# Kernel tuning notes

Hardware: AMD Instinct MI355X
Metric: run time of the kernel (lower is better)

## Reference

```python
import jax, jax.numpy as jnp
import numpy as np

B, T, D, V = 2, 2048, 768, 50257
REWARD_SCALE = 0.5
DIV_WEIGHT = 0.1
EPS = 1e-8  # torch cosine_similarity eps


def setup_inputs() -> dict:
    key = jax.random.key(0)
    k1, k2, k3, k4 = jax.random.split(key, 4)
    return {
        "pass2_hidden": jax.random.normal(k1, (B, T, D), dtype=jnp.float32),
        "pass3_hidden": jax.random.normal(k2, (B, T, D), dtype=jnp.float32),
        "W": jax.random.normal(k3, (V, D), dtype=jnp.float32) * 0.02,  # lm_head weight [V, D]
        "targets": jax.random.randint(k4, (B, T), 0, V, dtype=jnp.int64),
    }


def _masked_ce(hidden, W, targets):
    # hidden: [B,T,D], W: [V,D], targets: [B,T] with ignore_index=-1
    logits = jnp.einsum('btd,vd->btv', hidden, W).reshape(B * T, V)
    t = targets.reshape(B * T)
    valid = t != -1
    safe_t = jnp.where(valid, t, 0)
    logp = jax.nn.log_softmax(logits, axis=-1)
    nll = -jnp.take_along_axis(logp, safe_t[:, None], axis=-1)[:, 0]
    nll = jnp.where(valid, nll, 0.0)
    return nll.sum() / jnp.maximum(valid.sum(), 1).astype(nll.dtype)


def reference(pass2_hidden, pass3_hidden, W, targets):
    # pass 2 CE computed under no_grad in the original
    loss_p2 = jax.lax.stop_gradient(_masked_ce(pass2_hidden, W, targets))
    loss_p3 = _masked_ce(pass3_hidden, W, targets)
    reward_loss = -REWARD_SCALE * (loss_p2 - loss_p3)

    p2 = jax.lax.stop_gradient(pass2_hidden.reshape(B * T, D))  # .detach()
    p3 = pass3_hidden.reshape(B * T, D)
    n2 = jnp.maximum(jnp.linalg.norm(p2, axis=-1), EPS)
    n3 = jnp.maximum(jnp.linalg.norm(p3, axis=-1), EPS)
    cos = jnp.sum(p2 * p3, axis=-1) / (n2 * n3)
    divergence_loss = DIV_WEIGHT * cos.mean()
    return reward_loss + divergence_loss
```

## Files before the change

### kernel.cpp

```cpp
#include <hip/hip_runtime.h>
#include <math.h>

#define BT     4096
#define M_TOT  8192
#define KDIM   768
#define VDIM   50257
#define NBLK   393
#define NB256  197
#define KCH    24
#define KT     12
#define REWARD_SCALE 0.5
#define DIV_WEIGHT   0.1
#define EPS_COS      1e-8f
#define LOG2E        1.44269504088896340736f

typedef _Float16 half8 __attribute__((ext_vector_type(8)));
typedef float    f32x4 __attribute__((ext_vector_type(4)));

#define A_FRAGS (64*KCH*8*64)
#define W_FRAGS (NBLK*KCH*8*64)

__device__ __forceinline__ void g2l16(const short* g, short* l) {
    __builtin_amdgcn_global_load_lds(
        (const __attribute__((address_space(1))) unsigned int*)(const void*)g,
        (__attribute__((address_space(3))) unsigned int*)(void*)l,
        16, 0, 0);
}

__global__ __launch_bounds__(256)
void convert_A_kernel(const float* __restrict__ p2, const float* __restrict__ p3,
                      short* __restrict__ Ahi)
{
    __shared__ float Ls[128][36];
    const int mb = blockIdx.x;
    const int k0 = blockIdx.y;
    const int tid = threadIdx.x;

#pragma unroll
    for (int p = 0; p < 4; ++p) {
        int i = p * 1024 + tid * 4;
        int r = i >> 5;
        int c = i & 31;
        int m = mb * 128 + r;
        const float* src = (m < BT) ? (p2 + (size_t)m * KDIM)
                                    : (p3 + (size_t)(m - BT) * KDIM);
        float4 v = *(const float4*)(src + k0 * 32 + c);
        *(float4*)&Ls[r][c] = v;
    }
    __syncthreads();

    size_t base = ((size_t)(mb * KCH + k0) * 8) * 64;
#pragma unroll
    for (int h = 0; h < 2; ++h) {
        int f    = tid + h * 256;
        int lane = f & 63;
        int tile = f >> 6;
        int row  = tile * 16 + (lane & 15);
        int kq   = (lane >> 4) * 8;
        half8 out;
#pragma unroll
        for (int j = 0; j < 8; ++j) out[j] = (_Float16)Ls[row][kq + j];
        *(half8*)(Ahi + (base + f) * 8) = out;
    }
}

__global__ __launch_bounds__(256)
void convert_W_kernel(const float* __restrict__ W, short* __restrict__ Whi)
{
    __shared__ float Ls[128][36];
    const int nb = blockIdx.x;
    const int k0 = blockIdx.y;
    const int tid = threadIdx.x;

#pragma unroll
    for (int p = 0; p < 4; ++p) {
        int i = p * 1024 + tid * 4;
        int r = i >> 5;
        int c = i & 31;
        int v = nb * 128 + r;
        float4 val = make_float4(0.f, 0.f, 0.f, 0.f);
        if (v < VDIM) val = *(const float4*)(W + (size_t)v * KDIM + k0 * 32 + c);
        *(float4*)&Ls[r][c] = val;
    }
    __syncthreads();

    size_t base = ((size_t)(nb * KCH + k0) * 8) * 64;
#pragma unroll
    for (int h = 0; h < 2; ++h) {
        int f    = tid + h * 256;
        int lane = f & 63;
        int tile = f >> 6;
        int row  = tile * 16 + (lane & 15);
        int kq   = (lane >> 4) * 8;
        half8 out;
#pragma unroll
        for (int j = 0; j < 8; ++j) out[j] = (_Float16)(Ls[row][kq + j] * LOG2E);
        *(half8*)(Whi + (base + f) * 8) = out;
    }
}

#define BARRIER()  asm volatile("s_barrier" ::: "memory")
#define WAITV(n_)  asm volatile("s_waitcnt vmcnt(" #n_ ")" ::: "memory")
#define SB0()      __builtin_amdgcn_sched_barrier(0)

__global__ __launch_bounds__(512, 2)
void gemm_f16_kernel(const short* __restrict__ Ahi, const short* __restrict__ Whi,
                     double* __restrict__ g_sumexp)
{
    __shared__ __align__(16) short As[2][32][64][8];
    __shared__ __align__(16) short Bs[2][32][64][8];

    const int tid  = threadIdx.x;
    const int lane = tid & 63;
    const int w    = tid >> 6;
    const int wm   = w >> 2;
    const int wn   = w & 3;
    const int mb   = blockIdx.x;
    const int nb   = blockIdx.y;

    const int  f0       = (w & 3) * 4;
    const int  sh       = f0 >> 3;
    const int  tileBase = f0 & 7;
    const bool isB      = (w >= 4);
    const int  nb128    = min(2 * nb + sh, NBLK - 1);
    const short* gbase  = isB
        ? Whi + (size_t)nb128 * KCH * 4096 + lane * 8
        : Ahi + (size_t)(2 * mb + sh) * KCH * 4096 + lane * 8;
    short* stageL = (isB ? &Bs[0][0][0][0] : &As[0][0][0][0])
                    + lane * 8 + f0 * 512;

#define STAGEH(kc_, bufn_)                                                    \
    {                                                                         \
        short* l0 = stageL + ((bufn_) * 32 + ((kc_) & 1) * 16) * 512;         \
        const short* g0 = gbase + (size_t)((kc_) * 8 + tileBase) * 512;       \
        _Pragma("unroll")                                                     \
        for (int j = 0; j < 4; ++j) g2l16(g0 + j * 512, l0 + j * 512);        \
    }

    const short* aRd = &As[0][wm * 8][lane][0];
    const short* bRd = &Bs[0][(wn >> 1) * 8 + (wn & 1) * 4][lane][0];
#define RDA(CUR_, kh_, mh_, i_) \
    (*(const half8*)(aRd + ((CUR_) * 32 + (kh_) * 16 + (mh_) * 4 + (i_)) * 512))
#define RDB(CUR_, kh_, i_) \
    (*(const half8*)(bRd + ((CUR_) * 32 + (kh_) * 16 + (i_)) * 512))

    f32x4 acc[8][4];
#pragma unroll
    for (int i = 0; i < 8; ++i)
#pragma unroll
        for (int j = 0; j < 4; ++j) acc[i][j] = (f32x4)0.0f;

#define MFMA16(mh_)                                                           \
    __builtin_amdgcn_s_setprio(1);                                            \
    _Pragma("unroll")                                                         \
    for (int mt = 0; mt < 4; ++mt)                                            \
        _Pragma("unroll")                                                     \
        for (int nt = 0; nt < 4; ++nt)                                        \
            acc[(mh_) * 4 + mt][nt] = __builtin_amdgcn_mfma_f32_16x16x32_f16( \
                a[mt], b[nt], acc[(mh_) * 4 + mt][nt], 0, 0, 0);              \
    __builtin_amdgcn_s_setprio(0);

#define KTILE(kt_, CUR_, STG_, LAST_)                                         \
    {                                                                         \
        half8 a[4], b[4];                                                     \
                  \
        if (STG_) {                                                           \
            STAGEH(2 * ((kt_) + 1), (CUR_) ^ 1);                              \
            SB0();                                                            \
            STAGEH(2 * ((kt_) + 1) + 1, (CUR_) ^ 1);                          \
        }                                                                     \
        _Pragma("unroll")                                                     \
        for (int i = 0; i < 4; ++i) {                                         \
            a[i] = RDA(CUR_, 0, 0, i);                                        \
            b[i] = RDB(CUR_, 0, i);                                           \
        }                                                                     \
        BARRIER(); SB0();                                                     \
        MFMA16(0);                                                            \
        SB0(); BARRIER();                                                     \
                                                                      \
        _Pragma("unroll")                                                     \
        for (int i = 0; i < 4; ++i) a[i] = RDA(CUR_, 0, 1, i);                \
        BARRIER(); SB0();                                                     \
        MFMA16(1);                                                            \
        SB0();                                                                \
        if (LAST_) { WAITV(0); } else { WAITV(8); }                           \
        BARRIER();                                                            \
                                                                      \
        _Pragma("unroll")                                                     \
        for (int i = 0; i < 4; ++i) {                                         \
            a[i] = RDA(CUR_, 1, 0, i);                                        \
            b[i] = RDB(CUR_, 1, i);                                           \
        }                                                                     \
        BARRIER(); SB0();                                                     \
        MFMA16(0);                                                            \
        SB0(); BARRIER();                                                     \
                                                                      \
        _Pragma("unroll")                                                     \
        for (int i = 0; i < 4; ++i) a[i] = RDA(CUR_, 1, 1, i);                \
        BARRIER(); SB0();                                                     \
        MFMA16(1);                                                            \
        SB0();                                                                \
        if (!(LAST_)) { WAITV(4); }                                           \
        BARRIER();                                                            \
    }

    STAGEH(0, 0);
    SB0();
    STAGEH(1, 0);
    WAITV(4);
    BARRIER();

#pragma unroll 1
    for (int kt = 0; kt < 10; kt += 2) {
        KTILE(kt,     0, 1, 0)
        KTILE(kt + 1, 1, 1, 0)
    }
    KTILE(10, 0, 1, 0)
    KTILE(11, 1, 0, 1)

#undef KTILE
#undef MFMA16
#undef RDA
#undef RDB
#undef STAGEH

    __syncthreads();
    float* rowsum = (float*)&As[0][0][0][0];
    if (tid < 256) rowsum[tid] = 0.0f;
    __syncthreads();

    const int colBase = nb * 256 + wn * 64;
    const int quad = lane >> 4;
    const int cidx = lane & 15;
#pragma unroll
    for (int mt = 0; mt < 8; ++mt) {
#pragma unroll
        for (int r = 0; r < 4; ++r) {
            float s = 0.0f;
#pragma unroll
            for (int nt = 0; nt < 4; ++nt) {
                int col = colBase + nt * 16 + cidx;
                if (col < VDIM) s += __builtin_amdgcn_exp2f(acc[mt][nt][r]);
            }
            s += __shfl_xor(s, 1);
            s += __shfl_xor(s, 2);
            s += __shfl_xor(s, 4);
            s += __shfl_xor(s, 8);
            if (cidx == 0) {
                int row = wm * 128 + mt * 16 + quad * 4 + r;
                atomicAdd(&rowsum[row], s);
            }
        }
    }
    __syncthreads();
    if (tid < 256) {
        atomicAdd(&g_sumexp[(size_t)mb * 256 + tid], (double)rowsum[tid]);
    }
}

#define BM 128
#define BN 128
#define BK 16
#define LDPAD 4
__global__ __launch_bounds__(256)
void logits_expsum_kernel(const float* __restrict__ p2,
                          const float* __restrict__ p3,
                          const float* __restrict__ W,
                          double* __restrict__ g_sumexp)
{
    __shared__ float As[BK][BM + LDPAD];
    __shared__ float Bsh[BK][BN + LDPAD];
    __shared__ float rowsum[BM];

    const int tid     = threadIdx.x;
    const int rowBase = blockIdx.y * BM;
    const int colBase = blockIdx.x * BN;

    if (tid < BM) rowsum[tid] = 0.0f;

    float acc[8][8];
#pragma unroll
    for (int i = 0; i < 8; ++i)
#pragma unroll
        for (int j = 0; j < 8; ++j) acc[i][j] = 0.0f;

    const int ty = tid >> 4;
    const int tx = tid & 15;
    const int r0 = ty * 8;
    const int c0 = tx * 4;

    for (int k0 = 0; k0 < KDIM; k0 += BK) {
        __syncthreads();
#pragma unroll
        for (int l = 0; l < 2; ++l) {
            int id  = tid + l * 256;
            int row = id >> 2;
            int kq  = id & 3;
            int m   = rowBase + row;
            const float* src = (m < BT) ? (p2 + (size_t)m * KDIM)
                                        : (p3 + (size_t)(m - BT) * KDIM);
            float4 v = *(const float4*)(src + k0 + kq * 4);
            As[kq * 4 + 0][row] = v.x;
            As[kq * 4 + 1][row] = v.y;
            As[kq * 4 + 2][row] = v.z;
            As[kq * 4 + 3][row] = v.w;
        }
#pragma unroll
        for (int l = 0; l < 2; ++l) {
            int id  = tid + l * 256;
            int row = id >> 2;
            int kq  = id & 3;
            int c   = colBase + row;
            int cs  = (c < VDIM) ? c : (VDIM - 1);
            float4 v = *(const float4*)(W + (size_t)cs * KDIM + k0 + kq * 4);
            Bsh[kq * 4 + 0][row] = v.x;
            Bsh[kq * 4 + 1][row] = v.y;
            Bsh[kq * 4 + 2][row] = v.z;
            Bsh[kq * 4 + 3][row] = v.w;
        }
        __syncthreads();
#pragma unroll
        for (int kk = 0; kk < BK; ++kk) {
            float a[8], bb[8];
            *(float4*)&a[0]  = *(const float4*)&As[kk][r0];
            *(float4*)&a[4]  = *(const float4*)&As[kk][r0 + 4];
            *(float4*)&bb[0] = *(const float4*)&Bsh[kk][c0];
            *(float4*)&bb[4] = *(const float4*)&Bsh[kk][64 + c0];
#pragma unroll
            for (int i = 0; i < 8; ++i)
#pragma unroll
                for (int j = 0; j < 8; ++j)
                    acc[i][j] = fmaf(a[i], bb[j], acc[i][j]);
        }
    }

    __syncthreads();
#pragma unroll
    for (int i = 0; i < 8; ++i) {
        float s = 0.0f;
#pragma unroll
        for (int j = 0; j < 8; ++j) {
            int c = colBase + ((j < 4) ? (c0 + j) : (64 + c0 + (j - 4)));
            if (c < VDIM) s += expf(acc[i][j]);
        }
        atomicAdd(&rowsum[r0 + i], s);
    }
    __syncthreads();
    if (tid < BM) {
        atomicAdd(&g_sumexp[rowBase + tid], (double)rowsum[tid]);
    }
}

__global__ __launch_bounds__(256)
void finalize_tokens_kernel(const float* __restrict__ p2,
                            const float* __restrict__ p3,
                            const float* __restrict__ W,
                            const int*   __restrict__ targets,
                            const double* __restrict__ g_sumexp,
                            double* __restrict__ tokvals)
{
    const int t   = blockIdx.x;
    const int tid = threadIdx.x;
    const int tg  = targets[t];
    const bool valid = (tg >= 0);
    const float* w = W + (size_t)(valid ? tg : 0) * KDIM;
    const float* a = p2 + (size_t)t * KDIM;
    const float* b = p3 + (size_t)t * KDIM;

    float s22 = 0.f, s33 = 0.f, s23 = 0.f, s2w = 0.f, s3w = 0.f;
    for (int i = tid; i < KDIM; i += 256) {
        float x = a[i], y = b[i], ww = w[i];
        s22 = fmaf(x, x, s22);
        s33 = fmaf(y, y, s33);
        s23 = fmaf(x, y, s23);
        s2w = fmaf(x, ww, s2w);
        s3w = fmaf(y, ww, s3w);
    }
#pragma unroll
    for (int off = 32; off > 0; off >>= 1) {
        s22 += __shfl_down(s22, off);
        s33 += __shfl_down(s33, off);
        s23 += __shfl_down(s23, off);
        s2w += __shfl_down(s2w, off);
        s3w += __shfl_down(s3w, off);
    }
    __shared__ float sm[5][4];
    const int wv = tid >> 6, lane = tid & 63;
    if (lane == 0) {
        sm[0][wv] = s22; sm[1][wv] = s33; sm[2][wv] = s23;
        sm[3][wv] = s2w; sm[4][wv] = s3w;
    }
    __syncthreads();
    if (tid == 0) {
        float S22 = sm[0][0] + sm[0][1] + sm[0][2] + sm[0][3];
        float S33 = sm[1][0] + sm[1][1] + sm[1][2] + sm[1][3];
        float S23 = sm[2][0] + sm[2][1] + sm[2][2] + sm[2][3];
        float S2w = sm[3][0] + sm[3][1] + sm[3][2] + sm[3][3];
        float S3w = sm[4][0] + sm[4][1] + sm[4][2] + sm[4][3];

        float n2 = fmaxf(sqrtf(S22), EPS_COS);
        float n3 = fmaxf(sqrtf(S33), EPS_COS);

        double4 out;
        out.x = valid ? (log(g_sumexp[t])      - (double)S2w) : 0.0;
        out.y = valid ? (log(g_sumexp[BT + t]) - (double)S3w) : 0.0;
        out.z = (double)(S23 / (n2 * n3));
        out.w = valid ? 1.0 : 0.0;
        *(double4*)(tokvals + 4 * (size_t)t) = out;
    }
}

__global__ __launch_bounds__(1024)
void final_scalar_kernel(const double* __restrict__ tokvals,
                         float* __restrict__ out)
{
    const int tid = threadIdx.x;
    double s0 = 0.0, s1 = 0.0, s2 = 0.0, s3 = 0.0;
    for (int t = tid; t < BT; t += 1024) {
        double4 v = *(const double4*)(tokvals + 4 * (size_t)t);
        s0 += v.x; s1 += v.y; s2 += v.z; s3 += v.w;
    }
#pragma unroll
    for (int off = 32; off > 0; off >>= 1) {
        s0 += __shfl_down(s0, off);
        s1 += __shfl_down(s1, off);
        s2 += __shfl_down(s2, off);
        s3 += __shfl_down(s3, off);
    }
    __shared__ double sm[4][16];
    const int wv = tid >> 6, lane = tid & 63;
    if (lane == 0) { sm[0][wv] = s0; sm[1][wv] = s1; sm[2][wv] = s2; sm[3][wv] = s3; }
    __syncthreads();
    if (tid == 0) {
        double S0 = 0, S1 = 0, S2 = 0, S3 = 0;
#pragma unroll
        for (int i = 0; i < 16; ++i) { S0 += sm[0][i]; S1 += sm[1][i]; S2 += sm[2][i]; S3 += sm[3][i]; }
        double cnt = (S3 > 0.0) ? S3 : 1.0;
        double loss_p2 = S0 / cnt;
        double loss_p3 = S1 / cnt;
        double reward_loss = -REWARD_SCALE * (loss_p2 - loss_p3);
        double divergence  =  DIV_WEIGHT * (S2 / (double)BT);
        out[0] = (float)(reward_loss + divergence);
    }
}

extern "C" void kernel_launch(void* const* d_in, const int* in_sizes, int n_in,
                              void* d_out, int out_size, void* d_ws, size_t ws_size,
                              hipStream_t stream)
{
    const float* p2  = (const float*)d_in[0];
    const float* p3  = (const float*)d_in[1];
    const float* W   = (const float*)d_in[2];
    const int*   tgt = (const int*)d_in[3];

    double* g_sumexp = (double*)d_ws;
    double* tokvals  = g_sumexp + M_TOT;
    char*   fragbase = (char*)d_ws + 196608;

    hipMemsetAsync(d_ws, 0, 65536, stream);

    const size_t need = 196608 + (size_t)A_FRAGS * 16 + (size_t)W_FRAGS * 16;
    if (ws_size >= need) {
        short* Ahi = (short*)fragbase;
        short* Whi = Ahi + (size_t)A_FRAGS * 8;

        convert_A_kernel<<<dim3(64, KCH), dim3(256), 0, stream>>>(p2, p3, Ahi);
        convert_W_kernel<<<dim3(NBLK, KCH), dim3(256), 0, stream>>>(W, Whi);
        gemm_f16_kernel<<<dim3(32, NB256), dim3(512), 0, stream>>>(Ahi, Whi, g_sumexp);
    } else {
        logits_expsum_kernel<<<dim3(NBLK, 64), dim3(256), 0, stream>>>(p2, p3, W, g_sumexp);
    }

    finalize_tokens_kernel<<<dim3(BT), dim3(256), 0, stream>>>(
        p2, p3, W, tgt, g_sumexp, tokvals);

    final_scalar_kernel<<<dim3(1), dim3(1024), 0, stream>>>(tokvals, (float*)d_out);
}
```

Before: 925.7 us.

## Load W fragments directly into registers, drop B LDS staging and barriers

```diff
diff --git a/kernel.cpp b/kernel.cpp
--- a/kernel.cpp
+++ b/kernel.cpp
@@ -108,7 +108,6 @@
                      double* __restrict__ g_sumexp)
 {
     __shared__ __align__(16) short As[2][32][64][8];
-    __shared__ __align__(16) short Bs[2][32][64][8];
 
     const int tid  = threadIdx.x;
     const int lane = tid & 63;
@@ -118,111 +117,91 @@
     const int mb   = blockIdx.x;
     const int nb   = blockIdx.y;
 
-    const int  f0       = (w & 3) * 4;
-    const int  sh       = f0 >> 3;
-    const int  tileBase = f0 & 7;
-    const bool isB      = (w >= 4);
-    const int  nb128    = min(2 * nb + sh, NBLK - 1);
-    const short* gbase  = isB
-        ? Whi + (size_t)nb128 * KCH * 4096 + lane * 8
-        : Ahi + (size_t)(2 * mb + sh) * KCH * 4096 + lane * 8;
-    short* stageL = (isB ? &Bs[0][0][0][0] : &As[0][0][0][0])
-                    + lane * 8 + f0 * 512;
-
-#define STAGEH(kc_, bufn_)                                                    \
+    const int stc = w >> 2;
+    const int sth = (w >> 1) & 1;
+    const int stt = (w & 1) * 4;
+    const short* gA = Ahi + (size_t)(2 * mb + sth) * KCH * 4096 + lane * 8;
+    short* stageL = &As[0][0][0][0] + (stc * 16 + sth * 8 + stt) * 512 + lane * 8;
+
+    const short* aRd = &As[0][wm * 8][lane][0];
+
+    const int nb128 = (2 * nb + (wn >> 1) < NBLK) ? (2 * nb + (wn >> 1)) : (NBLK - 1);
+    const short* Bbase = Whi + (size_t)nb128 * KCH * 4096
+                             + (size_t)((wn & 1) * 4) * 512 + lane * 8;
+
+    f32x4 acc[8][4];
+#pragma unroll
+    for (int i = 0; i < 8; ++i)
+#pragma unroll
+        for (int j = 0; j < 4; ++j) acc[i][j] = (f32x4)0.0f;
+
+    half8 bE[2][4], bO[2][4];
+
+#define KTILE(kt_, CUR_, BC_, BN_, STG_, LAST_)                               \
     {                                                                         \
-        short* l0 = stageL + ((bufn_) * 32 + ((kc_) & 1) * 16) * 512;         \
-        const short* g0 = gbase + (size_t)((kc_) * 8 + tileBase) * 512;       \
-        _Pragma("unroll")                                                     \
-        for (int j = 0; j < 4; ++j) g2l16(g0 + j * 512, l0 + j * 512);        \
-    }
-
-    const short* aRd = &As[0][wm * 8][lane][0];
-    const short* bRd = &Bs[0][(wn >> 1) * 8 + (wn & 1) * 4][lane][0];
-#define RDA(CUR_, kh_, mh_, i_) \
-    (*(const half8*)(aRd + ((CUR_) * 32 + (kh_) * 16 + (mh_) * 4 + (i_)) * 512))
-#define RDB(CUR_, kh_, i_) \
-    (*(const half8*)(bRd + ((CUR_) * 32 + (kh_) * 16 + (i_)) * 512))
-
-    f32x4 acc[8][4];
-#pragma unroll
-    for (int i = 0; i < 8; ++i)
-#pragma unroll
-        for (int j = 0; j < 4; ++j) acc[i][j] = (f32x4)0.0f;
-
-#define MFMA16(mh_)                                                           \
-    __builtin_amdgcn_s_setprio(1);                                            \
-    _Pragma("unroll")                                                         \
-    for (int mt = 0; mt < 4; ++mt)                                            \
-        _Pragma("unroll")                                                     \
-        for (int nt = 0; nt < 4; ++nt)                                        \
-            acc[(mh_) * 4 + mt][nt] = __builtin_amdgcn_mfma_f32_16x16x32_f16( \
-                a[mt], b[nt], acc[(mh_) * 4 + mt][nt], 0, 0, 0);              \
-    __builtin_amdgcn_s_setprio(0);
-
-#define KTILE(kt_, CUR_, STG_, LAST_)                                         \
-    {                                                                         \
-        half8 a[4], b[4];                                                     \
-                  \
         if (STG_) {                                                           \
-            STAGEH(2 * ((kt_) + 1), (CUR_) ^ 1);                              \
+            _Pragma("unroll")                                                 \
+            for (int j = 0; j < 4; ++j)                                       \
+                g2l16(gA + (size_t)(((kt_) + 1) * 2 + stc) * 4096             \
+                         + (size_t)(stt + j) * 512,                           \
+                      stageL + (((CUR_) ^ 1) * 16384) + j * 512);             \
             SB0();                                                            \
-            STAGEH(2 * ((kt_) + 1) + 1, (CUR_) ^ 1);                          \
+            _Pragma("unroll")                                                 \
+            for (int c = 0; c < 2; ++c)                                       \
+                _Pragma("unroll")                                             \
+                for (int t = 0; t < 4; ++t)                                   \
+                    BN_[c][t] = *(const half8*)(Bbase                         \
+                        + (size_t)(((kt_) + 1) * 2 + c) * 4096 + t * 512);    \
+            SB0();                                                            \
         }                                                                     \
         _Pragma("unroll")                                                     \
-        for (int i = 0; i < 4; ++i) {                                         \
-            a[i] = RDA(CUR_, 0, 0, i);                                        \
-            b[i] = RDB(CUR_, 0, i);                                           \
+        for (int ph = 0; ph < 4; ++ph) {                                      \
+            const int c  = ph >> 1;                                           \
+            const int mh = ph & 1;                                            \
+            half8 a[4];                                                       \
+            _Pragma("unroll")                                                 \
+            for (int i = 0; i < 4; ++i)                                       \
+                a[i] = *(const half8*)(aRd                                    \
+                        + ((CUR_) * 32 + c * 16 + mh * 4 + i) * 512);         \
+            __builtin_amdgcn_s_setprio(1);                                    \
+            _Pragma("unroll")                                                 \
+            for (int mt = 0; mt < 4; ++mt)                                    \
+                _Pragma("unroll")                                             \
+                for (int nt = 0; nt < 4; ++nt)                                \
+                    acc[mh * 4 + mt][nt] =                                    \
+                        __builtin_amdgcn_mfma_f32_16x16x32_f16(               \
+                            a[mt], BC_[c][nt], acc[mh * 4 + mt][nt], 0, 0, 0);\
+            __builtin_amdgcn_s_setprio(0);                                    \
         }                                                                     \
-        BARRIER(); SB0();                                                     \
-        MFMA16(0);                                                            \
-        SB0(); BARRIER();                                                     \
-                                                                      \
-        _Pragma("unroll")                                                     \
-        for (int i = 0; i < 4; ++i) a[i] = RDA(CUR_, 0, 1, i);                \
-        BARRIER(); SB0();                                                     \
-        MFMA16(1);                                                            \
-        SB0();                                                                \
-        if (LAST_) { WAITV(0); } else { WAITV(8); }                           \
-        BARRIER();                                                            \
-                                                                      \
-        _Pragma("unroll")                                                     \
-        for (int i = 0; i < 4; ++i) {                                         \
-            a[i] = RDA(CUR_, 1, 0, i);                                        \
-            b[i] = RDB(CUR_, 1, i);                                           \
+        if (!(LAST_)) {                                                       \
+            WAITV(8);       \
+            BARRIER();                                                        \
         }                                                                     \
-        BARRIER(); SB0();                                                     \
-        MFMA16(0);                                                            \
-        SB0(); BARRIER();                                                     \
-                                                                      \
-        _Pragma("unroll")                                                     \
-        for (int i = 0; i < 4; ++i) a[i] = RDA(CUR_, 1, 1, i);                \
-        BARRIER(); SB0();                                                     \
-        MFMA16(1);                                                            \
-        SB0();                                                                \
-        if (!(LAST_)) { WAITV(4); }                                           \
-        BARRIER();                                                            \
-    }
-
-    STAGEH(0, 0);
+    }
+
+#pragma unroll
+    for (int j = 0; j < 4; ++j)
+        g2l16(gA + (size_t)stc * 4096 + (size_t)(stt + j) * 512,
+              stageL + j * 512);
     SB0();
-    STAGEH(1, 0);
-    WAITV(4);
+#pragma unroll
+    for (int c = 0; c < 2; ++c)
+#pragma unroll
+        for (int t = 0; t < 4; ++t)
+            bE[c][t] = *(const half8*)(Bbase + (size_t)c * 4096 + t * 512);
+    SB0();
+    WAITV(8);
     BARRIER();
 
 #pragma unroll 1
     for (int kt = 0; kt < 10; kt += 2) {
-        KTILE(kt,     0, 1, 0)
-        KTILE(kt + 1, 1, 1, 0)
-    }
-    KTILE(10, 0, 1, 0)
-    KTILE(11, 1, 0, 1)
+        KTILE(kt,     0, bE, bO, 1, 0)
+        KTILE(kt + 1, 1, bO, bE, 1, 0)
+    }
+    KTILE(10, 0, bE, bO, 1, 0)
+    KTILE(11, 1, bO, bE, 0, 1)
 
 #undef KTILE
-#undef MFMA16
-#undef RDA
-#undef RDB
-#undef STAGEH
 
     __syncthreads();
     float* rowsum = (float*)&As[0][0][0][0];
```

Result: slower. 970.2 us (+4.8%).
